# Performance work log

Hardware: AMD Instinct MI355X
Metric: run time of the kernel (lower is better)

The kernel has to match this reference:

```python
import jax, jax.numpy as jnp
import numpy as np
import math

B, N = 8, 131072
IN_C, OUT_C, STYLE_DIM, K = 64, 64, 256, 1
EPS = 1e-08


def setup_inputs() -> dict:
    key = jax.random.key(0)
    k1, k2, k3, k4 = jax.random.split(key, 4)
    x = jax.random.normal(k1, (B, N, IN_C), dtype=jnp.float32)
    style = jax.random.normal(k2, (B, STYLE_DIM), dtype=jnp.float32)
    # main conv weight: torch stores (1, out_c, in_c, k, k); k=1 -> (out_c, in_c)
    weight = jax.random.normal(k3, (OUT_C, IN_C), dtype=jnp.float32)
    bias = jnp.zeros((OUT_C,), dtype=jnp.float32)
    # EqualLinear modulation: weight (in_c, style_dim), bias init 0 -> style*scale+0, then +1
    mod_weight = jax.random.normal(k4, (IN_C, STYLE_DIM), dtype=jnp.float32)
    mod_bias = jnp.zeros((IN_C,), dtype=jnp.float32)
    return {"x": x, "style": style, "weight": weight, "bias": bias,
            "mod_weight": mod_weight, "mod_bias": mod_bias}


def reference(x, style, weight, bias, mod_weight, mod_bias):
    scale = 1.0 / math.sqrt(IN_C * K * K)          # conv weight scale
    mod_scale = 1.0 / math.sqrt(STYLE_DIM)         # EqualLinear scale (lr_mul=1)
    # modulation: EqualLinear(style) + 1  -> (b, in_c)
    s = style @ (mod_weight * mod_scale).T + mod_bias + 1.0
    # per-sample modulated weight: (b, out_c, in_c)
    w = scale * weight[None, :, :] * s[:, None, :]
    # demodulate over (in_c, k, k); k=1 so just in_c
    demod = jax.lax.rsqrt(jnp.sum(w * w, axis=2) + EPS)  # (b, out_c)
    w = w * demod[:, :, None]
    # grouped 1x1 conv == per-sample matmul over points: (b, n, out_c)
    out = jnp.einsum('bni,boi->bno', x, w) + bias[None, None, :]
    return out
```

## Files before the change

kernel.cpp:

```cpp
#include <hip/hip_runtime.h>
#include <hip/hip_bf16.h>

#define B_  8
#define N_  131072
#define C_  64
#define SD_ 256

typedef __attribute__((ext_vector_type(8))) short  short8;
typedef __attribute__((ext_vector_type(4))) float  floatx4;

static __device__ inline short bf16_of(float f) {
    __hip_bfloat16 h = __float2bfloat16(f);
    return *reinterpret_cast<short*>(&h);
}

__global__ void modw_kernel(const float* __restrict__ style,
                            const float* __restrict__ weight,
                            const float* __restrict__ mod_weight,
                            const float* __restrict__ mod_bias,
                            __hip_bfloat16* __restrict__ wout) {
    const int b = blockIdx.x;
    const int t = threadIdx.x;
    __shared__ float part[4][64];
    __shared__ float s_sh[64];

    const int i   = t & 63;
    const int seg = t >> 6;
    {
        const float* st = style + b * SD_ + seg * 64;
        const float* mw = mod_weight + i * SD_ + seg * 64;
        float p = 0.f;
        #pragma unroll
        for (int d = 0; d < 64; ++d) p += st[d] * mw[d];
        part[seg][i] = p;
    }
    __syncthreads();
    if (t < 64) {
        float s = (part[0][t] + part[1][t] + part[2][t] + part[3][t]) * 0.0625f
                  + mod_bias[t] + 1.0f;
        s_sh[t] = s;
    }
    __syncthreads();
    if (t < 64) {
        const int o = t;
        float wt[64];
        float sumsq = 0.f;
        #pragma unroll
        for (int ii = 0; ii < 64; ++ii) {
            float v = 0.125f * weight[o * 64 + ii] * s_sh[ii];
            wt[ii] = v;
            sumsq += v * v;
        }
        const float demod = rsqrtf(sumsq + 1e-8f);
        #pragma unroll
        for (int ii = 0; ii < 64; ++ii)
            wout[(b * 64 + o) * 64 + ii] = __float2bfloat16(wt[ii] * demod);
    }
}

__global__ __launch_bounds__(256) void conv_kernel(
        const float* __restrict__ x,
        const __hip_bfloat16* __restrict__ wmod,
        const float* __restrict__ bias,
        float* __restrict__ out) {
    const int lane = threadIdx.x & 63;
    const int wid  = threadIdx.x >> 6;
    const int gw   = blockIdx.x * 4 + wid;
    const int b    = gw >> 11;
    const int p0   = (gw & 2047) * 64;
    const int row  = lane & 15;
    const int quad = lane >> 4;

    short8 bf[4][2];
    const short* wb = (const short*)(wmod) + b * 64 * 64;
    #pragma unroll
    for (int nt = 0; nt < 4; ++nt)
        #pragma unroll
        for (int ks = 0; ks < 2; ++ks)
            bf[nt][ks] = *(const short8*)(wb + (nt * 16 + row) * 64 + ks * 32 + quad * 8);

    float bias_v[4];
    #pragma unroll
    for (int nt = 0; nt < 4; ++nt) bias_v[nt] = bias[nt * 16 + row];

    const size_t base = ((size_t)b * N_ + p0) * C_;
    const float* xb = x + base;
    float*       ob = out + base;

    #pragma unroll
    for (int pt = 0; pt < 4; ++pt) {
        const float* xr = xb + (pt * 16 + row) * C_ + quad * 8;
        floatx4 a0 = *(const floatx4*)(xr);
        floatx4 a1 = *(const floatx4*)(xr + 4);
        floatx4 a2 = *(const floatx4*)(xr + 32);
        floatx4 a3 = *(const floatx4*)(xr + 36);

        short8 af0, af1;
        #pragma unroll
        for (int j = 0; j < 4; ++j) {
            af0[j]     = bf16_of(a0[j]);
            af0[j + 4] = bf16_of(a1[j]);
            af1[j]     = bf16_of(a2[j]);
            af1[j + 4] = bf16_of(a3[j]);
        }

        floatx4 acc[4];
        #pragma unroll
        for (int nt = 0; nt < 4; ++nt) {
            acc[nt] = (floatx4){bias_v[nt], bias_v[nt], bias_v[nt], bias_v[nt]};
            acc[nt] = __builtin_amdgcn_mfma_f32_16x16x32_bf16(af0, bf[nt][0], acc[nt], 0, 0, 0);
            acc[nt] = __builtin_amdgcn_mfma_f32_16x16x32_bf16(af1, bf[nt][1], acc[nt], 0, 0, 0);
        }

        #pragma unroll
        for (int nt = 0; nt < 4; ++nt)
            #pragma unroll
            for (int r = 0; r < 4; ++r)
                ob[(pt * 16 + quad * 4 + r) * C_ + nt * 16 + row] = acc[nt][r];
    }
}

extern "C" void kernel_launch(void* const* d_in, const int* in_sizes, int n_in,
                              void* d_out, int out_size, void* d_ws, size_t ws_size,
                              hipStream_t stream) {
    const float* x          = (const float*)d_in[0];
    const float* style      = (const float*)d_in[1];
    const float* weight     = (const float*)d_in[2];
    const float* bias       = (const float*)d_in[3];
    const float* mod_weight = (const float*)d_in[4];
    const float* mod_bias   = (const float*)d_in[5];
    float* out = (float*)d_out;
    __hip_bfloat16* wmod = (__hip_bfloat16*)d_ws;

    modw_kernel<<<dim3(B_), dim3(256), 0, stream>>>(style, weight, mod_weight, mod_bias, wmod);
    conv_kernel<<<dim3((B_ * N_) / 256), dim3(256), 0, stream>>>(x, wmod, bias, out);
}
```

Baseline: 450.3 us.

## Swap MFMA operands for vectorized stores, nontemporal IO, and double points per wave

Swaps the A/B operands of the MFMA so each lane ends up holding four consecutive output channels of one point. The output can then be written as a single 16-byte nontemporal store instead of scattered scalar stores. Loads of x also become nontemporal, and each wave now processes 128 points instead of 64, with the grid halved to match. The aim is better write coalescing and less cache pollution in a bandwidth-bound kernel, at the cost of fewer blocks and possibly less latency hiding.

```diff
diff --git a/kernel.cpp b/kernel.cpp
--- a/kernel.cpp
+++ b/kernel.cpp
@@ -66,57 +66,53 @@
     const int lane = threadIdx.x & 63;
     const int wid  = threadIdx.x >> 6;
     const int gw   = blockIdx.x * 4 + wid;
-    const int b    = gw >> 11;
-    const int p0   = (gw & 2047) * 64;
+    const int b    = gw >> 10;
+    const int p0   = (gw & 1023) * 128;
     const int row  = lane & 15;
     const int quad = lane >> 4;
 
-    short8 bf[4][2];
-    const short* wb = (const short*)(wmod) + b * 64 * 64;
+    short8 wf[4][2];
+    const short* wb = (const short*)(wmod) + b * C_ * C_;
     #pragma unroll
-    for (int nt = 0; nt < 4; ++nt)
+    for (int ct = 0; ct < 4; ++ct)
         #pragma unroll
         for (int ks = 0; ks < 2; ++ks)
-            bf[nt][ks] = *(const short8*)(wb + (nt * 16 + row) * 64 + ks * 32 + quad * 8);
+            wf[ct][ks] = *(const short8*)(wb + (ct * 16 + row) * C_ + ks * 32 + quad * 8);
 
-    float bias_v[4];
+    floatx4 bias_v[4];
     #pragma unroll
-    for (int nt = 0; nt < 4; ++nt) bias_v[nt] = bias[nt * 16 + row];
+    for (int ct = 0; ct < 4; ++ct)
+        bias_v[ct] = *(const floatx4*)(bias + ct * 16 + quad * 4);
 
     const size_t base = ((size_t)b * N_ + p0) * C_;
     const float* xb = x + base;
     float*       ob = out + base;
 
-    #pragma unroll
-    for (int pt = 0; pt < 4; ++pt) {
+    #pragma unroll 2
+    for (int pt = 0; pt < 8; ++pt) {
         const float* xr = xb + (pt * 16 + row) * C_ + quad * 8;
-        floatx4 a0 = *(const floatx4*)(xr);
-        floatx4 a1 = *(const floatx4*)(xr + 4);
-        floatx4 a2 = *(const floatx4*)(xr + 32);
-        floatx4 a3 = *(const floatx4*)(xr + 36);
+        floatx4 a0 = __builtin_nontemporal_load((const floatx4*)xr);
+        floatx4 a1 = __builtin_nontemporal_load((const floatx4*)(xr + 4));
+        floatx4 a2 = __builtin_nontemporal_load((const floatx4*)(xr + 32));
+        floatx4 a3 = __builtin_nontemporal_load((const floatx4*)(xr + 36));
 
-        short8 af0, af1;
+        short8 xf0, xf1;
         #pragma unroll
         for (int j = 0; j < 4; ++j) {
-            af0[j]     = bf16_of(a0[j]);
-            af0[j + 4] = bf16_of(a1[j]);
-            af1[j]     = bf16_of(a2[j]);
-            af1[j + 4] = bf16_of(a3[j]);
+            xf0[j]     = bf16_of(a0[j]);
+            xf0[j + 4] = bf16_of(a1[j]);
+            xf1[j]     = bf16_of(a2[j]);
+            xf1[j + 4] = bf16_of(a3[j]);
         }
 
-        floatx4 acc[4];
+        float* orow = ob + (pt * 16 + row) * C_ + quad * 4;
         #pragma unroll
-        for (int nt = 0; nt < 4; ++nt) {
-            acc[nt] = (floatx4){bias_v[nt], bias_v[nt], bias_v[nt], bias_v[nt]};
-            acc[nt] = __builtin_amdgcn_mfma_f32_16x16x32_bf16(af0, bf[nt][0], acc[nt], 0, 0, 0);
-            acc[nt] = __builtin_amdgcn_mfma_f32_16x16x32_bf16(af1, bf[nt][1], acc[nt], 0, 0, 0);
+        for (int ct = 0; ct < 4; ++ct) {
+            floatx4 acc = bias_v[ct];
+            acc = __builtin_amdgcn_mfma_f32_16x16x32_bf16(wf[ct][0], xf0, acc, 0, 0, 0);
+            acc = __builtin_amdgcn_mfma_f32_16x16x32_bf16(wf[ct][1], xf1, acc, 0, 0, 0);
+            __builtin_nontemporal_store(acc, (floatx4*)(orow + ct * 16));
         }
-
-        #pragma unroll
-        for (int nt = 0; nt < 4; ++nt)
-            #pragma unroll
-            for (int r = 0; r < 4; ++r)
-                ob[(pt * 16 + quad * 4 + r) * C_ + nt * 16 + row] = acc[nt][r];
     }
 }
 
@@ -133,5 +129,5 @@
     __hip_bfloat16* wmod = (__hip_bfloat16*)d_ws;
 
     modw_kernel<<<dim3(B_), dim3(256), 0, stream>>>(style, weight, mod_weight, mod_bias, wmod);
-    conv_kernel<<<dim3((B_ * N_) / 256), dim3(256), 0, stream>>>(x, wmod, bias, out);
+    conv_kernel<<<dim3((B_ * N_) / (128 * 4)), dim3(256), 0, stream>>>(x, wmod, bias, out);
 }
```

Measured after the change: 469.0 us. +4.2%, slower.
